# Kernel tuning notes

Hardware: AMD Instinct MI355X
Metric: run time of the kernel (lower is better)

Reference implementation:

```python
import jax, jax.numpy as jnp
import numpy as np

HIDDEN = 64
OUT = 16
NEG = 1e12


def sinusoidal_pos(seq_len, dim, dtype=jnp.float32):
    # kexue.fm SinusoidalPositionEmbedding, merge_mode='zero': [1, S, dim]
    pos = jnp.arange(seq_len, dtype=dtype)[:, None]            # [S,1]
    idx = jnp.arange(dim // 2, dtype=dtype)
    inv_freq = jnp.power(10000.0, -2.0 * idx / dim)            # [dim/2]
    ang = pos * inv_freq[None, :]                              # [S, dim/2]
    emb = jnp.stack([jnp.sin(ang), jnp.cos(ang)], axis=-1)     # [S, dim/2, 2]
    return emb.reshape(seq_len, dim)[None]                     # [1, S, dim]; ::2 = sin, 1::2 = cos


def rotate_half_interleaved(x):
    # result[...,2i] = -x[...,2i+1]; result[...,2i+1] = x[...,2i]
    return jnp.stack([-x[..., 1::2], x[..., ::2]], axis=-1).reshape(x.shape)


def setup_inputs() -> dict:
    key = jax.random.key(0)
    ks = jax.random.split(key, 5)
    B, S, D = 4, 1024, 768
    inputs = jax.random.normal(ks[0], (B, S, D), dtype=jnp.float32)
    mask = jnp.ones((B, S), dtype=jnp.float32)
    W1 = jax.random.normal(ks[1], (D, 2 * HIDDEN), dtype=jnp.float32) * 0.02
    b1 = jax.random.normal(ks[2], (2 * HIDDEN,), dtype=jnp.float32) * 0.02
    W2 = jax.random.normal(ks[3], (2 * HIDDEN, 2 * OUT), dtype=jnp.float32) * 0.02
    b2 = jax.random.normal(ks[4], (2 * OUT,), dtype=jnp.float32) * 0.02
    return {"inputs": inputs, "mask": mask, "W1": W1, "b1": b1, "W2": W2, "b2": b2}


def reference(inputs, mask, W1, b1, W2, b2):
    B, S, _ = inputs.shape
    h = inputs @ W1 + b1                       # [B,S,2H]
    qw, kw = h[..., ::2], h[..., 1::2]         # [B,S,H] each

    pos = sinusoidal_pos(S, HIDDEN, h.dtype)   # [1,S,H]
    cos_pos = jnp.tile(pos[..., 1::2], (1, 1, 2))   # .repeat(1,1,2) tiles, not interleaves
    sin_pos = jnp.tile(pos[..., ::2], (1, 1, 2))
    qw = qw * cos_pos + rotate_half_interleaved(qw) * sin_pos
    kw = kw * cos_pos + rotate_half_interleaved(kw) * sin_pos

    logits = jnp.einsum('bmd,bnd->bmn', qw, kw) / jnp.sqrt(jnp.asarray(HIDDEN, h.dtype))
    bias = jnp.einsum('bnh->bhn', h @ W2 + b2) / 2.0        # [B,2*OUT,S]
    logits = logits[:, None] + bias[:, ::2, None, :] + bias[:, 1::2, :, None]  # [B,OUT,S,S]

    pad = mask[:, None, None, :]                            # broadcast over heads and query dim
    pad = jnp.broadcast_to(pad, (B, OUT, S, S))
    logits = logits * pad - (1.0 - pad) * NEG

    tril = jnp.tril(jnp.ones((S, S), dtype=logits.dtype), -1)
    logits = logits - tril * NEG
    return logits
```

## Files before the change

### kernel.cpp

```cpp
#include <hip/hip_runtime.h>
#include <math.h>

#define NEGV 1000000000000.0f
#define LDSTR 68

__global__ __launch_bounds__(256) void k1_fused(
    const float* __restrict__ x,
    const float* __restrict__ W1,
    const float* __restrict__ b1,
    const float* __restrict__ W2,
    const float* __restrict__ b2,
    float* __restrict__ qw,
    float* __restrict__ kw,
    float* __restrict__ bias)
{
    __shared__ float hs[16][128];
    const int t    = threadIdx.x;
    const int row0 = blockIdx.x * 16;
    const int j    = t & 127;
    const int rh = __builtin_amdgcn_readfirstlane((int)threadIdx.x) >> 7;

    float acc[8] = {0.f,0.f,0.f,0.f,0.f,0.f,0.f,0.f};
    #pragma unroll 4
    for (int k = 0; k < 768; ++k) {
        const float w = W1[k * 128 + j];
        #pragma unroll
        for (int r = 0; r < 8; ++r)
            acc[r] = fmaf(x[(size_t)(row0 + 2*r + rh) * 768 + k], w, acc[r]);
    }
    const float bj = b1[j];
    #pragma unroll
    for (int r = 0; r < 8; ++r) hs[2*r + rh][j] = acc[r] + bj;
    __syncthreads();

    for (int idx = t; idx < 16 * 64; idx += 256) {
        const int r = idx >> 6, c = idx & 63;
        const int rowg = row0 + r;
        const int s = rowg & 1023;
        const int f = c & 31;
        const float invf = exp2f(-0.4152410118609203f * (float)f);
        const float ang = (float)s * invf;
        float sn, cs;
        sincosf(ang, &sn, &cs);
        const int   pc  = (c & 1) ? (c - 1) : (c + 1);
        const float sgn = (c & 1) ? sn : -sn;
        const float qv = fmaf(hs[r][2*c],     cs, hs[r][2*pc]     * sgn);
        const float kv = fmaf(hs[r][2*c + 1], cs, hs[r][2*pc + 1] * sgn);
        qw[(size_t)rowg * 64 + c] = qv;
        kw[(size_t)rowg * 64 + c] = kv;
    }

    for (int idx = t; idx < 16 * 32; idx += 256) {
        const int r = idx >> 5, c = idx & 31;
        const int rowg = row0 + r;
        const int s = rowg & 1023, bb = rowg >> 10;
        float a = 0.f;
        #pragma unroll 4
        for (int k = 0; k < 128; ++k)
            a = fmaf(hs[r][k], W2[k * 32 + c], a);
        bias[(size_t)(bb * 32 + c) * 1024 + s] = (a + b2[c]) * 0.5f;
    }
}

__global__ __launch_bounds__(256) void k2_outer(
    const float* __restrict__ qw, const float* __restrict__ kw,
    const float* __restrict__ bias, const float* __restrict__ mask,
    float* __restrict__ out)
{
    __shared__ float qs[64 * LDSTR];
    __shared__ float ks[64 * LDSTR];
    __shared__ float bA[16][64];
    __shared__ float bB[16][64];
    __shared__ float padv[64];

    const int t  = threadIdx.x;
    const int n0 = blockIdx.x * 64;
    const int m0 = blockIdx.y * 64;
    const int b  = blockIdx.z;

    const float4* qg = (const float4*)(qw + (size_t)(b * 1024 + m0) * 64);
    const float4* kg = (const float4*)(kw + (size_t)(b * 1024 + n0) * 64);
    #pragma unroll
    for (int it = 0; it < 4; ++it) {
        const int idx = t + it * 256;
        const int m = idx >> 4, kgp = idx & 15;
        float4 v = qg[idx];
        qs[(4*kgp + 0) * LDSTR + m] = v.x;
        qs[(4*kgp + 1) * LDSTR + m] = v.y;
        qs[(4*kgp + 2) * LDSTR + m] = v.z;
        qs[(4*kgp + 3) * LDSTR + m] = v.w;
        v = kg[idx];
        ks[(4*kgp + 0) * LDSTR + m] = v.x;
        ks[(4*kgp + 1) * LDSTR + m] = v.y;
        ks[(4*kgp + 2) * LDSTR + m] = v.z;
        ks[(4*kgp + 3) * LDSTR + m] = v.w;
    }
    for (int idx = t; idx < 16 * 64; idx += 256) {
        const int o = idx >> 6, c = idx & 63;
        bA[o][c] = bias[(size_t)(b * 32 + 2*o)     * 1024 + n0 + c];
        bB[o][c] = bias[(size_t)(b * 32 + 2*o + 1) * 1024 + m0 + c];
    }
    if (t < 64) padv[t] = mask[b * 1024 + n0 + t];
    __syncthreads();

    const int tn = t & 15, tm = t >> 4;
    float acc[4][4];
    #pragma unroll
    for (int i = 0; i < 4; ++i)
        #pragma unroll
        for (int c = 0; c < 4; ++c) acc[i][c] = 0.f;

    #pragma unroll 8
    for (int k = 0; k < 64; ++k) {
        const float4 qv = *(const float4*)&qs[k * LDSTR + 4 * tm];
        const float4 kv = *(const float4*)&ks[k * LDSTR + 4 * tn];
        const float qa[4] = {qv.x, qv.y, qv.z, qv.w};
        const float ka[4] = {kv.x, kv.y, kv.z, kv.w};
        #pragma unroll
        for (int i = 0; i < 4; ++i)
            #pragma unroll
            for (int c = 0; c < 4; ++c)
                acc[i][c] = fmaf(qa[i], ka[c], acc[i][c]);
    }

    const float4 pv = *(const float4*)&padv[4 * tn];
    const float p[4] = {pv.x, pv.y, pv.z, pv.w};
    float negterm[4];
    #pragma unroll
    for (int c = 0; c < 4; ++c) negterm[c] = (1.f - p[c]) * NEGV;
    const int ng = n0 + 4 * tn;

    #pragma unroll
    for (int o = 0; o < 16; ++o) {
        const float4 av = *(const float4*)&bA[o][4 * tn];
        const float a[4] = {av.x, av.y, av.z, av.w};
        #pragma unroll
        for (int i = 0; i < 4; ++i) {
            const int mg = m0 + 4 * tm + i;
            const float vb = bB[o][4 * tm + i];
            float rv[4];
            #pragma unroll
            for (int c = 0; c < 4; ++c) {
                float v = fmaf(acc[i][c], 0.125f, a[c] + vb);
                v = v * p[c] - negterm[c];
                if (ng + c < mg) v -= NEGV;
                rv[c] = v;
            }
            float4 r4; r4.x = rv[0]; r4.y = rv[1]; r4.z = rv[2]; r4.w = rv[3];
            *(float4*)(out + ((size_t)((b * 16 + o) * 1024 + mg)) * 1024 + ng) = r4;
        }
    }
}

extern "C" void kernel_launch(void* const* d_in, const int* in_sizes, int n_in,
                              void* d_out, int out_size, void* d_ws, size_t ws_size,
                              hipStream_t stream) {
    const float* x    = (const float*)d_in[0];
    const float* mask = (const float*)d_in[1];
    const float* W1   = (const float*)d_in[2];
    const float* b1   = (const float*)d_in[3];
    const float* W2   = (const float*)d_in[4];
    const float* b2   = (const float*)d_in[5];
    float* out = (float*)d_out;

    float* ws   = (float*)d_ws;
    float* qw   = ws;
    float* kw   = ws + 4096 * 64;
    float* bias = ws + 2 * 4096 * 64;

    hipLaunchKernelGGL(k1_fused, dim3(256), dim3(256), 0, stream,
                       x, W1, b1, W2, b2, qw, kw, bias);
    hipLaunchKernelGGL(k2_outer, dim3(16, 16, 4), dim3(256), 0, stream,
                       qw, kw, bias, mask, out);
}
```

Baseline: 412.3 us.

## Stage x rows in LDS and use float4 register tiling in first GEMM

The first kernel now loads its 16 input rows into shared memory with coalesced float4 loads. Each thread then computes a 2x4 output tile, reading W1 as float4 and x from LDS, instead of each thread streaming x from global memory per k. This targets redundant global x reads and scalar W1 loads in the projection GEMM. It uses about 50KB of shared memory per block, which may limit occupancy, and k1 is likely a small share of the total time next to the output-bound k2.

```diff
diff --git a/kernel.cpp b/kernel.cpp
--- a/kernel.cpp
+++ b/kernel.cpp
@@ -14,23 +14,53 @@
     float* __restrict__ kw,
     float* __restrict__ bias)
 {
-    __shared__ float hs[16][128];
+    __shared__ float xs[16][772];
+    __shared__ float hs[16][132];
     const int t    = threadIdx.x;
     const int row0 = blockIdx.x * 16;
-    const int j    = t & 127;
-    const int rh = __builtin_amdgcn_readfirstlane((int)threadIdx.x) >> 7;
-
-    float acc[8] = {0.f,0.f,0.f,0.f,0.f,0.f,0.f,0.f};
-    #pragma unroll 4
-    for (int k = 0; k < 768; ++k) {
-        const float w = W1[k * 128 + j];
-        #pragma unroll
-        for (int r = 0; r < 8; ++r)
-            acc[r] = fmaf(x[(size_t)(row0 + 2*r + rh) * 768 + k], w, acc[r]);
-    }
-    const float bj = b1[j];
-    #pragma unroll
-    for (int r = 0; r < 8; ++r) hs[2*r + rh][j] = acc[r] + bj;
+
+    {
+        const float4* xg = (const float4*)(x + (size_t)row0 * 768);
+        #pragma unroll
+        for (int it = 0; it < 12; ++it) {
+            const int idx = t + it * 256;
+            const int r = idx / 192, c4 = idx - r * 192;
+            const float4 v = xg[idx];
+            *(float4*)&xs[r][c4 * 4] = v;
+        }
+    }
+    __syncthreads();
+
+    const int jc = (t & 31) * 4;
+    const int rg = (t >> 5) * 2;
+    float accA[4] = {0.f,0.f,0.f,0.f};
+    float accB[4] = {0.f,0.f,0.f,0.f};
+    #pragma unroll 2
+    for (int k = 0; k < 768; k += 4) {
+        const float4 xa = *(const float4*)&xs[rg][k];
+        const float4 xb = *(const float4*)&xs[rg + 1][k];
+        const float xav[4] = {xa.x, xa.y, xa.z, xa.w};
+        const float xbv[4] = {xb.x, xb.y, xb.z, xb.w};
+        #pragma unroll
+        for (int kk = 0; kk < 4; ++kk) {
+            const float4 w = *(const float4*)&W1[(size_t)(k + kk) * 128 + jc];
+            const float wv[4] = {w.x, w.y, w.z, w.w};
+            #pragma unroll
+            for (int c = 0; c < 4; ++c) {
+                accA[c] = fmaf(xav[kk], wv[c], accA[c]);
+                accB[c] = fmaf(xbv[kk], wv[c], accB[c]);
+            }
+        }
+    }
+    {
+        const float4 bv = *(const float4*)&b1[jc];
+        const float bvv[4] = {bv.x, bv.y, bv.z, bv.w};
+        #pragma unroll
+        for (int c = 0; c < 4; ++c) {
+            hs[rg][jc + c]     = accA[c] + bvv[c];
+            hs[rg + 1][jc + c] = accB[c] + bvv[c];
+        }
+    }
     __syncthreads();
 
     for (int idx = t; idx < 16 * 64; idx += 256) {
```

Measured after the change: 359.0 us. 12.9% less time.
